# Performance work log

Hardware: AMD Instinct MI355X
Metric: run time of the kernel (lower is better)

Reference implementation:

```python
import jax, jax.numpy as jnp
import numpy as np

EMBED_DIM = 768
NUM_HEADS = 12
HEAD_DIM = EMBED_DIM // NUM_HEADS


def setup_inputs() -> dict:
    key = jax.random.key(0)
    k1, k2, k3 = jax.random.split(key, 3)
    B, T = 128, 128
    x = jax.random.normal(k1, (B, T, EMBED_DIM), dtype=jnp.float32)
    # weights stored as [in, out] so forward is x @ W (equivalent to torch Linear, bias=False)
    w_qkv = jax.random.normal(k2, (EMBED_DIM, 3 * EMBED_DIM), dtype=jnp.float32) * (EMBED_DIM ** -0.5)
    w_proj = jax.random.normal(k3, (EMBED_DIM, EMBED_DIM), dtype=jnp.float32) * (EMBED_DIM ** -0.5)
    return {"x": x, "w_qkv": w_qkv, "w_proj": w_proj}


def reference(x, w_qkv, w_proj):
    B, T, C = x.shape
    # fused QKV projection -> (3, B, H, T, D)
    qkv = (x @ w_qkv).reshape(B, T, 3, NUM_HEADS, HEAD_DIM)
    q, k, v = jnp.transpose(qkv, (2, 0, 3, 1, 4))
    # scaled dot-product scores (B, H, T, T)
    att = jnp.einsum('bhqd,bhkd->bhqk', q, k) * (HEAD_DIM ** -0.5)
    causal = jnp.tril(jnp.ones((T, T), dtype=bool))
    att = jnp.where(causal, att, -jnp.inf)
    # float32 softmax then cast back (matches att.float().softmax().to(x.dtype))
    att = jax.nn.softmax(att.astype(jnp.float32), axis=-1).astype(x.dtype)
    # dropout is identity in eval/reference mode
    out = jnp.einsum('bhqk,bhkd->bhqd', att, v)          # (B, H, T, D)
    out = jnp.transpose(out, (0, 2, 1, 3)).reshape(B, T, C)
    return out @ w_proj
```

## Files before the change

### kernel.cpp

```cpp
#include <hip/hip_runtime.h>

typedef __bf16 bf16_t;
typedef bf16_t bf16x8 __attribute__((ext_vector_type(8)));
typedef bf16_t bf16x4 __attribute__((ext_vector_type(4)));
typedef float f32x4 __attribute__((ext_vector_type(4)));

__device__ __forceinline__ f32x4 mfma16(bf16x8 a, bf16x8 b, f32x4 c) {
  return __builtin_amdgcn_mfma_f32_16x16x32_bf16(a, b, c, 0, 0, 0);
}

__device__ __forceinline__ void gload16(const bf16_t* g, bf16_t* l) {
  __builtin_amdgcn_global_load_lds(
      (const __attribute__((address_space(1))) void*)g,
      (__attribute__((address_space(3))) void*)l, 16, 0, 0);
}

__global__ void prep_kernel(const float* __restrict__ x, const float* __restrict__ wq,
                            const float* __restrict__ wp, bf16_t* __restrict__ xb,
                            bf16_t* __restrict__ wqt, bf16_t* __restrict__ wpt) {
  __shared__ bf16_t tile[32][33];
  const int bid = blockIdx.x;
  if (bid < 12288) {
    int i = bid * 256 + threadIdx.x;
    float4 v = ((const float4*)x)[i];
    bf16x4 o;
    o[0] = (bf16_t)v.x; o[1] = (bf16_t)v.y; o[2] = (bf16_t)v.z; o[3] = (bf16_t)v.w;
    *(bf16x4*)&xb[(size_t)i * 4] = o;
    return;
  }
  const int t = bid - 12288;
  const int ty = t / 96, txb = t % 96;
  const float* in;
  bf16_t* out;
  int N, n0;
  if (txb < 72) { in = wq; out = wqt; N = 2304; n0 = txb * 32; }
  else          { in = wp; out = wpt; N = 768;  n0 = (txb - 72) * 32; }
  const int k0 = ty * 32;
  const int tx = threadIdx.x & 31, tyy = threadIdx.x >> 5;
#pragma unroll
  for (int ph = 0; ph < 4; ++ph) {
    int k = tyy + ph * 8;
    tile[k][tx] = (bf16_t)in[(size_t)(k0 + k) * N + n0 + tx];
  }
  __syncthreads();
#pragma unroll
  for (int ph = 0; ph < 4; ++ph) {
    int n = tyy + ph * 8;
    out[(size_t)(n0 + n) * 768 + k0 + tx] = tile[tx][n];
  }
}

template <int BN, int MINW, bool F32OUT>
__global__ __launch_bounds__(256, MINW) void gemm_p32(
    const bf16_t* __restrict__ A, const bf16_t* __restrict__ Bt,
    void* __restrict__ Cout, int N, int nbn, int q, int r) {
  constexpr int K = 768;
  constexpr int NKT = 24;
  constexpr int NQ = BN / 32;
  __shared__ bf16_t As[2][128 * 32];
  __shared__ bf16_t Bs[2][BN * 32];
  const int tid = threadIdx.x;
  const int lane = tid & 63;
  const int w = tid >> 6;
  const int wm = w >> 1, wn = w & 1;
  const int lr = lane & 15, kg = lane >> 4;

  const int G = gridDim.x;
  const int bid = blockIdx.x;
  const int lb = (bid & 7) * (G >> 3) + (bid >> 3);
  int nj, start;
  if (lb < r) { nj = q + 1; start = lb * (q + 1); }
  else        { nj = q;     start = r * (q + 1) + (lb - r) * q; }

  auto stage = [&](int buf, const bf16_t* Aj, const bf16_t* Bj, int k0) {
#pragma unroll
    for (int it = 0; it < 2; ++it) {
      int c = it * 256 + tid;
      int rr = c >> 2, p = c & 3;
      gload16(Aj + (size_t)rr * K + (k0 + ((p ^ ((rr >> 1) & 3)) << 3)),
              &As[buf][c * 8]);
    }
#pragma unroll
    for (int it = 0; it < BN / 64; ++it) {
      int c = it * 256 + tid;
      int rr = c >> 2, p = c & 3;
      gload16(Bj + (size_t)rr * K + (k0 + ((p ^ ((rr >> 1) & 3)) << 3)),
              &Bs[buf][c * 8]);
    }
  };

  int job = start;
  int bm = job / nbn, bn = job - bm * nbn;
  const bf16_t* Aj = A + (size_t)bm * (128 * K);
  const bf16_t* Bj = Bt + (size_t)bn * (BN * K);
  stage(0, Aj, Bj, 0);
  __syncthreads();
  int buf = 0;

  const int ph = kg ^ ((lr >> 1) & 3);

  for (int j = 0; j < nj; ++j) {
    f32x4 acc[4][NQ];
#pragma unroll
    for (int i = 0; i < 4; ++i)
#pragma unroll
      for (int n = 0; n < NQ; ++n) acc[i][n] = (f32x4){0.f, 0.f, 0.f, 0.f};

    int nbm = 0, nbnx = 0;
    const bf16_t *nAj = nullptr, *nBj = nullptr;
    if (j + 1 < nj) {
      int njob = job + 1;
      nbm = njob / nbn; nbnx = njob - nbm * nbn;
      nAj = A + (size_t)nbm * (128 * K);
      nBj = Bt + (size_t)nbnx * (BN * K);
    }

    for (int kt = 0; kt < NKT; ++kt) {
      if (kt + 1 < NKT)     stage(buf ^ 1, Aj, Bj, (kt + 1) << 5);
      else if (j + 1 < nj)  stage(buf ^ 1, nAj, nBj, 0);

      bf16x8 af[4], bfv[NQ];
#pragma unroll
      for (int mq = 0; mq < 4; ++mq) {
        int rr = wm * 64 + mq * 16 + lr;
        af[mq] = *(const bf16x8*)&As[buf][(rr << 5) + (ph << 3)];
      }
#pragma unroll
      for (int nq = 0; nq < NQ; ++nq) {
        int rr = wn * (BN / 2) + nq * 16 + lr;
        bfv[nq] = *(const bf16x8*)&Bs[buf][(rr << 5) + (ph << 3)];
      }
#pragma unroll
      for (int mq = 0; mq < 4; ++mq)
#pragma unroll
        for (int nq = 0; nq < NQ; ++nq)
          acc[mq][nq] = mfma16(af[mq], bfv[nq], acc[mq][nq]);

      __syncthreads();
      buf ^= 1;
    }

    const int row0 = bm * 128 + wm * 64 + kg * 4;
    const int col0 = bn * BN + wn * (BN / 2) + lr;
#pragma unroll
    for (int mq = 0; mq < 4; ++mq)
#pragma unroll
      for (int nq = 0; nq < NQ; ++nq)
#pragma unroll
        for (int rr = 0; rr < 4; ++rr) {
          size_t idx = (size_t)(row0 + mq * 16 + rr) * N + (col0 + nq * 16);
          if constexpr (F32OUT)
            ((float*)Cout)[idx] = acc[mq][nq][rr];
          else
            ((bf16_t*)Cout)[idx] = (bf16_t)acc[mq][nq][rr];
        }

    job++; bm = nbm; bn = nbnx; Aj = nAj; Bj = nBj;
  }
}

#define ATT_H 12
__global__ __launch_bounds__(256, 2) void attn_kernel(const bf16_t* __restrict__ qkv,
                                                      bf16_t* __restrict__ obuf) {
  __shared__ bf16_t Ks[128 * 72];
  __shared__ bf16_t Vt[64 * 136];
  __shared__ bf16_t Ps[128 * 136];
  const int tid = threadIdx.x, lane = tid & 63, w = tid >> 6;
  const int lr = lane & 15, kg = lane >> 4;
  const int bh = blockIdx.x;
  const int b = bh / ATT_H, h = bh % ATT_H;
  const size_t base = (size_t)b * 128 * 2304;
  const int hoff = h * 64;

#pragma unroll
  for (int it = 0; it < 4; ++it) {
    int idx = it * 256 + tid;
    int r = idx >> 3, slot = idx & 7;
    bf16x8 v = *(const bf16x8*)&qkv[base + (size_t)r * 2304 + 768 + hoff + slot * 8];
    *(bf16x8*)&Ks[r * 72 + slot * 8] = v;
  }
#pragma unroll 4
  for (int it = 0; it < 32; ++it) {
    int idx = it * 256 + tid;
    int t = idx >> 6, d = idx & 63;
    Vt[d * 136 + t] = qkv[base + (size_t)t * 2304 + 1536 + hoff + d];
  }
  const int qrow0 = w * 32;
  bf16x8 qf[2][2];
#pragma unroll
  for (int mt = 0; mt < 2; ++mt)
#pragma unroll
    for (int kk = 0; kk < 2; ++kk)
      qf[mt][kk] = *(const bf16x8*)&qkv[base + (size_t)(qrow0 + mt * 16 + lr) * 2304 + hoff +
                                        kk * 32 + kg * 8];
  __syncthreads();

  const int NT = 2 * w + 2;
  f32x4 acc[2][8];
#pragma unroll
  for (int mt = 0; mt < 2; ++mt)
#pragma unroll
    for (int nt = 0; nt < 8; ++nt) acc[mt][nt] = (f32x4){0.f, 0.f, 0.f, 0.f};

#pragma unroll
  for (int nt = 0; nt < 8; ++nt) {
    if (nt < NT) {
#pragma unroll
      for (int kk = 0; kk < 2; ++kk) {
        bf16x8 kf = *(const bf16x8*)&Ks[(nt * 16 + lr) * 72 + kk * 32 + kg * 8];
        acc[0][nt] = mfma16(qf[0][kk], kf, acc[0][nt]);
        acc[1][nt] = mfma16(qf[1][kk], kf, acc[1][nt]);
      }
    }
  }

#pragma unroll
  for (int mt = 0; mt < 2; ++mt) {
#pragma unroll
    for (int rr = 0; rr < 4; ++rr) {
      const int row = qrow0 + mt * 16 + kg * 4 + rr;
      float m = -1e30f;
#pragma unroll
      for (int nt = 0; nt < 8; ++nt) {
        if (nt < NT) {
          int col = nt * 16 + lr;
          float sv = acc[mt][nt][rr] * 0.125f;
          sv = (col <= row) ? sv : -1e30f;
          acc[mt][nt][rr] = sv;
          m = fmaxf(m, sv);
        }
      }
      m = fmaxf(m, __shfl_xor(m, 1));
      m = fmaxf(m, __shfl_xor(m, 2));
      m = fmaxf(m, __shfl_xor(m, 4));
      m = fmaxf(m, __shfl_xor(m, 8));
      float ssum = 0.f;
#pragma unroll
      for (int nt = 0; nt < 8; ++nt) {
        if (nt < NT) {
          float p = __builtin_amdgcn_exp2f((acc[mt][nt][rr] - m) * 1.44269504f);
          acc[mt][nt][rr] = p;
          ssum += p;
        }
      }
      ssum += __shfl_xor(ssum, 1);
      ssum += __shfl_xor(ssum, 2);
      ssum += __shfl_xor(ssum, 4);
      ssum += __shfl_xor(ssum, 8);
      float inv = 1.0f / ssum;
#pragma unroll
      for (int nt = 0; nt < 8; ++nt) {
        if (nt < NT) Ps[row * 136 + nt * 16 + lr] = (bf16_t)(acc[mt][nt][rr] * inv);
      }
    }
  }

  f32x4 oacc[2][4];
#pragma unroll
  for (int mt = 0; mt < 2; ++mt)
#pragma unroll
    for (int dt = 0; dt < 4; ++dt) oacc[mt][dt] = (f32x4){0.f, 0.f, 0.f, 0.f};

  const int KS = w + 1;
#pragma unroll
  for (int ks = 0; ks < 4; ++ks) {
    if (ks < KS) {
      bf16x8 pa0 = *(const bf16x8*)&Ps[(qrow0 + lr) * 136 + ks * 32 + kg * 8];
      bf16x8 pa1 = *(const bf16x8*)&Ps[(qrow0 + 16 + lr) * 136 + ks * 32 + kg * 8];
#pragma unroll
      for (int dt = 0; dt < 4; ++dt) {
        bf16x8 vb = *(const bf16x8*)&Vt[(dt * 16 + lr) * 136 + ks * 32 + kg * 8];
        oacc[0][dt] = mfma16(pa0, vb, oacc[0][dt]);
        oacc[1][dt] = mfma16(pa1, vb, oacc[1][dt]);
      }
    }
  }

#pragma unroll
  for (int mt = 0; mt < 2; ++mt)
#pragma unroll
    for (int dt = 0; dt < 4; ++dt)
#pragma unroll
      for (int rr = 0; rr < 4; ++rr) {
        int t = qrow0 + mt * 16 + kg * 4 + rr;
        obuf[((size_t)b * 128 + t) * 768 + hoff + dt * 16 + lr] = (bf16_t)oacc[mt][dt][rr];
      }
}

extern "C" void kernel_launch(void* const* d_in, const int* in_sizes, int n_in,
                              void* d_out, int out_size, void* d_ws, size_t ws_size,
                              hipStream_t stream) {
  const float* x = (const float*)d_in[0];
  const float* w_qkv = (const float*)d_in[1];
  const float* w_proj = (const float*)d_in[2];
  float* out = (float*)d_out;
  char* ws = (char*)d_ws;

  bf16_t* xb     = (bf16_t*)(ws);
  bf16_t* wqkvt  = (bf16_t*)(ws + 25165824);
  bf16_t* wprojt = (bf16_t*)(ws + 28704768);
  bf16_t* qkv    = (bf16_t*)(ws + 29884416);
  bf16_t* obuf   = (bf16_t*)(ws + 105381888);

  prep_kernel<<<dim3(12288 + 2304), dim3(256), 0, stream>>>(x, w_qkv, w_proj, xb, wqkvt, wprojt);
  gemm_p32<128, 3, false><<<dim3(768), dim3(256), 0, stream>>>(
      xb, wqkvt, (void*)qkv, 2304, 18, 3, 0);
  attn_kernel<<<dim3(1536), dim3(256), 0, stream>>>(qkv, obuf);
  gemm_p32<64, 6, true><<<dim3(1536), dim3(256), 0, stream>>>(
      obuf, wprojt, (void*)out, 768, 12, 1, 0);
}
```

Baseline: 162.9 us.

## Fuse fp32-to-bf16 conversion of x into the QKV GEMM A-tile loads

New measurement: 159.4 us. 1.02x faster.

```diff
diff --git a/kernel.cpp b/kernel.cpp
--- a/kernel.cpp
+++ b/kernel.cpp
@@ -15,20 +15,10 @@
       (__attribute__((address_space(3))) void*)l, 16, 0, 0);
 }
 
-__global__ void prep_kernel(const float* __restrict__ x, const float* __restrict__ wq,
-                            const float* __restrict__ wp, bf16_t* __restrict__ xb,
-                            bf16_t* __restrict__ wqt, bf16_t* __restrict__ wpt) {
+__global__ void prepw_kernel(const float* __restrict__ wq, const float* __restrict__ wp,
+                             bf16_t* __restrict__ wqt, bf16_t* __restrict__ wpt) {
   __shared__ bf16_t tile[32][33];
-  const int bid = blockIdx.x;
-  if (bid < 12288) {
-    int i = bid * 256 + threadIdx.x;
-    float4 v = ((const float4*)x)[i];
-    bf16x4 o;
-    o[0] = (bf16_t)v.x; o[1] = (bf16_t)v.y; o[2] = (bf16_t)v.z; o[3] = (bf16_t)v.w;
-    *(bf16x4*)&xb[(size_t)i * 4] = o;
-    return;
-  }
-  const int t = bid - 12288;
+  const int t = blockIdx.x;
   const int ty = t / 96, txb = t % 96;
   const float* in;
   bf16_t* out;
@@ -50,15 +40,12 @@
   }
 }
 
-template <int BN, int MINW, bool F32OUT>
-__global__ __launch_bounds__(256, MINW) void gemm_p32(
-    const bf16_t* __restrict__ A, const bf16_t* __restrict__ Bt,
-    void* __restrict__ Cout, int N, int nbn, int q, int r) {
-  constexpr int K = 768;
-  constexpr int NKT = 24;
-  constexpr int NQ = BN / 32;
+__global__ __launch_bounds__(256, 3) void gemm1_fused(
+    const float* __restrict__ X, const bf16_t* __restrict__ Bt,
+    bf16_t* __restrict__ Cout) {
+  constexpr int K = 768, NKT = 24, NBN = 18, JPB = 3;
   __shared__ bf16_t As[2][128 * 32];
-  __shared__ bf16_t Bs[2][BN * 32];
+  __shared__ bf16_t Bs[2][128 * 32];
   const int tid = threadIdx.x;
   const int lane = tid & 63;
   const int w = tid >> 6;
@@ -68,95 +55,179 @@
   const int G = gridDim.x;
   const int bid = blockIdx.x;
   const int lb = (bid & 7) * (G >> 3) + (bid >> 3);
-  int nj, start;
-  if (lb < r) { nj = q + 1; start = lb * (q + 1); }
-  else        { nj = q;     start = r * (q + 1) + (lb - r) * q; }
-
-  auto stage = [&](int buf, const bf16_t* Aj, const bf16_t* Bj, int k0) {
+  const int start = lb * JPB;
+  const int bm = start / NBN;
+  const int bn0 = start - bm * NBN;
+  const float* Xj = X + (size_t)bm * (128 * K);
+
+  const int cA0 = tid, cA1 = 256 + tid;
+  const int rA0 = cA0 >> 2, pA0 = cA0 & 3;
+  const int rA1 = cA1 >> 2, pA1 = cA1 & 3;
+  const int sA0 = (pA0 ^ ((rA0 >> 1) & 3)) << 3;
+  const int sA1 = (pA1 ^ ((rA1 >> 1) & 3)) << 3;
+
+  float4 lv0a, lv0b, lv1a, lv1b;
+  auto loadA = [&](int k0) {
+    lv0a = *(const float4*)&Xj[(size_t)rA0 * K + k0 + sA0];
+    lv0b = *(const float4*)&Xj[(size_t)rA0 * K + k0 + sA0 + 4];
+    lv1a = *(const float4*)&Xj[(size_t)rA1 * K + k0 + sA1];
+    lv1b = *(const float4*)&Xj[(size_t)rA1 * K + k0 + sA1 + 4];
+  };
+  auto writeA = [&](int buf) {
+    bf16x8 o0, o1;
+    o0[0] = (bf16_t)lv0a.x; o0[1] = (bf16_t)lv0a.y; o0[2] = (bf16_t)lv0a.z; o0[3] = (bf16_t)lv0a.w;
+    o0[4] = (bf16_t)lv0b.x; o0[5] = (bf16_t)lv0b.y; o0[6] = (bf16_t)lv0b.z; o0[7] = (bf16_t)lv0b.w;
+    o1[0] = (bf16_t)lv1a.x; o1[1] = (bf16_t)lv1a.y; o1[2] = (bf16_t)lv1a.z; o1[3] = (bf16_t)lv1a.w;
+    o1[4] = (bf16_t)lv1b.x; o1[5] = (bf16_t)lv1b.y; o1[6] = (bf16_t)lv1b.z; o1[7] = (bf16_t)lv1b.w;
+    *(bf16x8*)&As[buf][cA0 * 8] = o0;
+    *(bf16x8*)&As[buf][cA1 * 8] = o1;
+  };
+  auto gloadB = [&](int buf, const bf16_t* Bj, int k0) {
 #pragma unroll
     for (int it = 0; it < 2; ++it) {
       int c = it * 256 + tid;
       int rr = c >> 2, p = c & 3;
-      gload16(Aj + (size_t)rr * K + (k0 + ((p ^ ((rr >> 1) & 3)) << 3)),
-              &As[buf][c * 8]);
-    }
-#pragma unroll
-    for (int it = 0; it < BN / 64; ++it) {
-      int c = it * 256 + tid;
-      int rr = c >> 2, p = c & 3;
-      gload16(Bj + (size_t)rr * K + (k0 + ((p ^ ((rr >> 1) & 3)) << 3)),
-              &Bs[buf][c * 8]);
+      gload16(Bj + (size_t)rr * K + (k0 + ((p ^ ((rr >> 1) & 3)) << 3)), &Bs[buf][c * 8]);
     }
   };
 
-  int job = start;
-  int bm = job / nbn, bn = job - bm * nbn;
-  const bf16_t* Aj = A + (size_t)bm * (128 * K);
-  const bf16_t* Bj = Bt + (size_t)bn * (BN * K);
-  stage(0, Aj, Bj, 0);
+  const int ph = kg ^ ((lr >> 1) & 3);
+
+  const bf16_t* Bj = Bt + (size_t)bn0 * (128 * K);
+  loadA(0);
+  gloadB(0, Bj, 0);
+  writeA(0);
   __syncthreads();
   int buf = 0;
 
-  const int ph = kg ^ ((lr >> 1) & 3);
-
-  for (int j = 0; j < nj; ++j) {
-    f32x4 acc[4][NQ];
+  for (int j = 0; j < JPB; ++j) {
+    f32x4 acc[4][4];
 #pragma unroll
     for (int i = 0; i < 4; ++i)
 #pragma unroll
-      for (int n = 0; n < NQ; ++n) acc[i][n] = (f32x4){0.f, 0.f, 0.f, 0.f};
-
-    int nbm = 0, nbnx = 0;
-    const bf16_t *nAj = nullptr, *nBj = nullptr;
-    if (j + 1 < nj) {
-      int njob = job + 1;
-      nbm = njob / nbn; nbnx = njob - nbm * nbn;
-      nAj = A + (size_t)nbm * (128 * K);
-      nBj = Bt + (size_t)nbnx * (BN * K);
-    }
+      for (int n = 0; n < 4; ++n) acc[i][n] = (f32x4){0.f, 0.f, 0.f, 0.f};
+
+    const int bn = bn0 + j;
+    const bf16_t* BjN = Bt + (size_t)(bn + 1) * (128 * K);
 
     for (int kt = 0; kt < NKT; ++kt) {
-      if (kt + 1 < NKT)     stage(buf ^ 1, Aj, Bj, (kt + 1) << 5);
-      else if (j + 1 < nj)  stage(buf ^ 1, nAj, nBj, 0);
-
-      bf16x8 af[4], bfv[NQ];
+      const bool haveNext = (kt + 1 < NKT) || (j + 1 < JPB);
+      const int nk0 = (kt + 1 < NKT) ? ((kt + 1) << 5) : 0;
+      const bf16_t* nBj = (kt + 1 < NKT) ? Bj : BjN;
+      if (haveNext) {
+        loadA(nk0);
+        gloadB(buf ^ 1, nBj, nk0);
+      }
+      bf16x8 af[4], bfv[4];
 #pragma unroll
       for (int mq = 0; mq < 4; ++mq) {
         int rr = wm * 64 + mq * 16 + lr;
         af[mq] = *(const bf16x8*)&As[buf][(rr << 5) + (ph << 3)];
       }
 #pragma unroll
-      for (int nq = 0; nq < NQ; ++nq) {
-        int rr = wn * (BN / 2) + nq * 16 + lr;
+      for (int nq = 0; nq < 4; ++nq) {
+        int rr = wn * 64 + nq * 16 + lr;
         bfv[nq] = *(const bf16x8*)&Bs[buf][(rr << 5) + (ph << 3)];
       }
 #pragma unroll
       for (int mq = 0; mq < 4; ++mq)
 #pragma unroll
-        for (int nq = 0; nq < NQ; ++nq)
+        for (int nq = 0; nq < 4; ++nq)
           acc[mq][nq] = mfma16(af[mq], bfv[nq], acc[mq][nq]);
 
+      if (haveNext) writeA(buf ^ 1);
       __syncthreads();
       buf ^= 1;
     }
 
     const int row0 = bm * 128 + wm * 64 + kg * 4;
-    const int col0 = bn * BN + wn * (BN / 2) + lr;
+    const int col0 = bn * 128 + wn * 64 + lr;
 #pragma unroll
     for (int mq = 0; mq < 4; ++mq)
 #pragma unroll
-      for (int nq = 0; nq < NQ; ++nq)
-#pragma unroll
-        for (int rr = 0; rr < 4; ++rr) {
-          size_t idx = (size_t)(row0 + mq * 16 + rr) * N + (col0 + nq * 16);
-          if constexpr (F32OUT)
-            ((float*)Cout)[idx] = acc[mq][nq][rr];
-          else
-            ((bf16_t*)Cout)[idx] = (bf16_t)acc[mq][nq][rr];
-        }
-
-    job++; bm = nbm; bn = nbnx; Aj = nAj; Bj = nBj;
-  }
+      for (int nq = 0; nq < 4; ++nq)
+#pragma unroll
+        for (int rr = 0; rr < 4; ++rr)
+          Cout[(size_t)(row0 + mq * 16 + rr) * 2304 + (col0 + nq * 16)] =
+              (bf16_t)acc[mq][nq][rr];
+
+    Bj = BjN;
+  }
+}
+
+__global__ __launch_bounds__(256, 3) void gemm2_kernel(
+    const bf16_t* __restrict__ A, const bf16_t* __restrict__ Bt,
+    float* __restrict__ Cout) {
+  constexpr int K = 768, NKT = 24, NBN = 6;
+  __shared__ bf16_t As[2][128 * 32];
+  __shared__ bf16_t Bs[2][128 * 32];
+  const int tid = threadIdx.x;
+  const int lane = tid & 63;
+  const int w = tid >> 6;
+  const int wm = w >> 1, wn = w & 1;
+  const int lr = lane & 15, kg = lane >> 4;
+
+  const int G = gridDim.x;
+  const int bid = blockIdx.x;
+  const int lb = (bid & 7) * (G >> 3) + (bid >> 3);
+  const int bm = lb / NBN, bn = lb - bm * NBN;
+  const bf16_t* Aj = A + (size_t)bm * (128 * K);
+  const bf16_t* Bj = Bt + (size_t)bn * (128 * K);
+
+  auto stage = [&](int buf, int k0) {
+#pragma unroll
+    for (int it = 0; it < 2; ++it) {
+      int c = it * 256 + tid;
+      int rr = c >> 2, p = c & 3;
+      int so = k0 + ((p ^ ((rr >> 1) & 3)) << 3);
+      gload16(Aj + (size_t)rr * K + so, &As[buf][c * 8]);
+      gload16(Bj + (size_t)rr * K + so, &Bs[buf][c * 8]);
+    }
+  };
+
+  stage(0, 0);
+  __syncthreads();
+  int buf = 0;
+
+  f32x4 acc[4][4];
+#pragma unroll
+  for (int i = 0; i < 4; ++i)
+#pragma unroll
+    for (int n = 0; n < 4; ++n) acc[i][n] = (f32x4){0.f, 0.f, 0.f, 0.f};
+
+  const int ph = kg ^ ((lr >> 1) & 3);
+
+  for (int kt = 0; kt < NKT; ++kt) {
+    if (kt + 1 < NKT) stage(buf ^ 1, (kt + 1) << 5);
+    bf16x8 af[4], bfv[4];
+#pragma unroll
+    for (int mq = 0; mq < 4; ++mq) {
+      int rr = wm * 64 + mq * 16 + lr;
+      af[mq] = *(const bf16x8*)&As[buf][(rr << 5) + (ph << 3)];
+    }
+#pragma unroll
+    for (int nq = 0; nq < 4; ++nq) {
+      int rr = wn * 64 + nq * 16 + lr;
+      bfv[nq] = *(const bf16x8*)&Bs[buf][(rr << 5) + (ph << 3)];
+    }
+#pragma unroll
+    for (int mq = 0; mq < 4; ++mq)
+#pragma unroll
+      for (int nq = 0; nq < 4; ++nq)
+        acc[mq][nq] = mfma16(af[mq], bfv[nq], acc[mq][nq]);
+    __syncthreads();
+    buf ^= 1;
+  }
+
+  const int row0 = bm * 128 + wm * 64 + kg * 4;
+  const int col0 = bn * 128 + wn * 64 + lr;
+#pragma unroll
+  for (int mq = 0; mq < 4; ++mq)
+#pragma unroll
+    for (int nq = 0; nq < 4; ++nq)
+#pragma unroll
+      for (int rr = 0; rr < 4; ++rr)
+        Cout[(size_t)(row0 + mq * 16 + rr) * 768 + (col0 + nq * 16)] = acc[mq][nq][rr];
 }
 
 #define ATT_H 12
@@ -296,16 +367,13 @@
   float* out = (float*)d_out;
   char* ws = (char*)d_ws;
 
-  bf16_t* xb     = (bf16_t*)(ws);
-  bf16_t* wqkvt  = (bf16_t*)(ws + 25165824);
-  bf16_t* wprojt = (bf16_t*)(ws + 28704768);
-  bf16_t* qkv    = (bf16_t*)(ws + 29884416);
-  bf16_t* obuf   = (bf16_t*)(ws + 105381888);
-
-  prep_kernel<<<dim3(12288 + 2304), dim3(256), 0, stream>>>(x, w_qkv, w_proj, xb, wqkvt, wprojt);
-  gemm_p32<128, 3, false><<<dim3(768), dim3(256), 0, stream>>>(
-      xb, wqkvt, (void*)qkv, 2304, 18, 3, 0);
+  bf16_t* wqkvt  = (bf16_t*)(ws);
+  bf16_t* wprojt = (bf16_t*)(ws + 3538944);
+  bf16_t* qkv    = (bf16_t*)(ws + 4718592);
+  bf16_t* obuf   = (bf16_t*)(ws + 80216064);
+
+  prepw_kernel<<<dim3(2304), dim3(256), 0, stream>>>(w_qkv, w_proj, wqkvt, wprojt);
+  gemm1_fused<<<dim3(768), dim3(256), 0, stream>>>(x, wqkvt, qkv);
   attn_kernel<<<dim3(1536), dim3(256), 0, stream>>>(qkv, obuf);
-  gemm_p32<64, 6, true><<<dim3(1536), dim3(256), 0, stream>>>(
-      obuf, wprojt, (void*)out, 768, 12, 1, 0);
-}
+  gemm2_kernel<<<dim3(768), dim3(256), 0, stream>>>(obuf, wprojt, out);
+}
```
